# Kernel tuning notes

Measured on AMD Instinct MI355X. Metric: run time of the kernel, lower is better.

The kernel has to match this reference:

```python
import jax, jax.numpy as jnp
import numpy as np

EMB = 1024
HEADS = 16
HEAD_DIM = EMB // HEADS


def setup_inputs() -> dict:
    key = jax.random.key(0)
    ks = jax.random.split(key, 11)
    B, S = 4, 2048
    scale = 1.0 / np.sqrt(EMB)
    inp = {
        "query": jax.random.normal(ks[0], (B, S, EMB), jnp.float32),
        "key": jax.random.normal(ks[1], (B, S, EMB), jnp.float32),
        "value": jax.random.normal(ks[2], (B, S, EMB), jnp.float32),
        "Wq": jax.random.normal(ks[3], (EMB, EMB), jnp.float32) * scale,
        "bq": jnp.zeros((EMB,), jnp.float32),
        "Wk": jax.random.normal(ks[4], (EMB, EMB), jnp.float32) * scale,
        "bk": jnp.zeros((EMB,), jnp.float32),
        "Wv": jax.random.normal(ks[5], (EMB, EMB), jnp.float32) * scale,
        "bv": jnp.zeros((EMB,), jnp.float32),
        "Wo": jax.random.normal(ks[6], (EMB, EMB), jnp.float32) * scale,
        "bo": jnp.zeros((EMB,), jnp.float32),
    }
    return inp


def reference(query, key, value, Wq, bq, Wk, bk, Wv, bv, Wo, bo):
    B, S, E = query.shape
    H, D = HEADS, HEAD_DIM

    def split_heads(x):  # [B,S,E] -> [B,H,S,D]
        return x.reshape(B, -1, H, D).transpose(0, 2, 1, 3)

    Q = split_heads(query @ Wq + bq)
    K = split_heads(key @ Wk + bk)
    V = split_heads(value @ Wv + bv)

    scores = jnp.einsum("bhqd,bhkd->bhqk", Q, K) / jnp.sqrt(jnp.float32(D))
    attn = jax.nn.softmax(scores, axis=-1)
    out = jnp.einsum("bhqk,bhkd->bhqd", attn, V)
    out = out.transpose(0, 2, 1, 3).reshape(B, S, E)
    return out @ Wo + bo
```

## Files before the change

### kernel.cpp

```cpp
#include <hip/hip_runtime.h>

typedef unsigned short ushort_t;
typedef __attribute__((ext_vector_type(8))) short bf16x8;
typedef __attribute__((ext_vector_type(4))) float f32x4;
typedef __attribute__((ext_vector_type(16))) float f32x16;
typedef __attribute__((ext_vector_type(4))) int i32x4;
typedef __attribute__((ext_vector_type(2))) unsigned int u32x2;

#define QSCALE 0.1803368801111204f

__device__ inline ushort_t f2bf(float f) {
    unsigned int u = __float_as_uint(f);
    unsigned int r = (u + 0x7FFFu + ((u >> 16) & 1u)) >> 16;
    return (ushort_t)r;
}
__device__ inline unsigned pkbf(float x, float y) {
    unsigned d;
    asm("v_cvt_pk_bf16_f32 %0, %1, %2" : "=v"(d) : "v"(x), "v"(y));
    return d;
}
__device__ inline bf16x8 frag_from(unsigned a, unsigned b, unsigned c, unsigned d) {
    union { i32x4 i; bf16x8 v; } u;
    u.i[0] = (int)a; u.i[1] = (int)b; u.i[2] = (int)c; u.i[3] = (int)d;
    return u.v;
}

__device__ inline bf16x8 mkfrag(float x0, float x1, float x2, float x3,
                                float x4, float x5, float x6, float x7, int hi) {
    unsigned A_ = pkbf(x0, x1), B_ = pkbf(x2, x3), C_ = pkbf(x4, x5), D_ = pkbf(x6, x7);
    unsigned Ax = (unsigned)__shfl_xor((int)A_, 32);
    unsigned Bx = (unsigned)__shfl_xor((int)B_, 32);
    unsigned Cx = (unsigned)__shfl_xor((int)C_, 32);
    unsigned Dx = (unsigned)__shfl_xor((int)D_, 32);
    return frag_from(hi ? Cx : A_, hi ? Dx : B_, hi ? C_ : Ax, hi ? D_ : Bx);
}

__global__ __launch_bounds__(256) void transpose_cast4(
    const float* __restrict__ W0, const float* __restrict__ W1,
    const float* __restrict__ W2, const float* __restrict__ W3,
    ushort_t* __restrict__ T0, ushort_t* __restrict__ T1,
    ushort_t* __restrict__ T2, ushort_t* __restrict__ T3) {
    __shared__ float tile[32][33];
    const int which = blockIdx.x >> 10;
    const float* W = which == 0 ? W0 : which == 1 ? W1 : which == 2 ? W2 : W3;
    ushort_t* Wt = which == 0 ? T0 : which == 1 ? T1 : which == 2 ? T2 : T3;
    const int bidx = blockIdx.x & 1023;
    const int bx = bidx & 31, by = bidx >> 5;
    const int n0 = bx * 32, k0 = by * 32;
    const int tx = threadIdx.x & 31, ty = threadIdx.x >> 5;
#pragma unroll
    for (int i = 0; i < 4; ++i) {
        int r = ty + i * 8;
        tile[r][tx] = W[(k0 + r) * 1024 + n0 + tx];
    }
    __syncthreads();
#pragma unroll
    for (int i = 0; i < 4; ++i) {
        int r = ty + i * 8;
        Wt[(n0 + r) * 1024 + k0 + tx] = f2bf(tile[tx][r]);
    }
}

__global__ __launch_bounds__(256) void v_transpose(const ushort_t* __restrict__ Vp,
                                                   ushort_t* __restrict__ Vt) {
    __shared__ alignas(16) ushort_t tile[64][72];
    const int bid = blockIdx.x;
    const int pair = bid >> 5, st0 = (bid & 31) * 64;
    const ushort_t* src = Vp + (size_t)pair * 2048 * 64;
    ushort_t* dst = Vt + (size_t)pair * 64 * 2048;
    const int t = threadIdx.x;
    const int sl = t >> 2, d0 = (t & 3) * 16;
    *(bf16x8*)&tile[sl][d0] = *(const bf16x8*)&src[(size_t)(st0 + sl) * 64 + d0];
    *(bf16x8*)&tile[sl][d0 + 8] = *(const bf16x8*)&src[(size_t)(st0 + sl) * 64 + d0 + 8];
    __syncthreads();
    const int dl = t >> 2, s0 = (t & 3) * 16;
    bf16x8 a, b;
#pragma unroll
    for (int j = 0; j < 8; ++j) {
        a[j] = (short)tile[s0 + j][dl];
        b[j] = (short)tile[s0 + 8 + j][dl];
    }
    *(bf16x8*)&dst[(size_t)dl * 2048 + st0 + s0] = a;
    *(bf16x8*)&dst[(size_t)dl * 2048 + st0 + s0 + 8] = b;
}

template <int AF32, int OMODE>
__global__ __launch_bounds__(256) void gemm_bt(const void* __restrict__ Ap,
                                               const ushort_t* __restrict__ Bt,
                                               const float* __restrict__ bias,
                                               void* __restrict__ out, float scale) {
    __shared__ alignas(16) ushort_t As[128 * 72];
    __shared__ alignas(16) ushort_t Bs[128 * 72];
    const int t = threadIdx.x;
    const int lane = t & 63, w = t >> 6;
    const int q = lane & 15, g = lane >> 4;
    const int wr = w >> 1, wc = w & 1;
    const int bm = blockIdx.x & 63, bn = blockIdx.x >> 6;
    const int m0 = bm * 128, n0 = bn * 128;

    f32x4 acc[4][4];
#pragma unroll
    for (int i = 0; i < 4; ++i)
#pragma unroll
        for (int j = 0; j < 4; ++j) acc[i][j] = (f32x4){0.f, 0.f, 0.f, 0.f};

    for (int k0 = 0; k0 < 1024; k0 += 64) {
        __syncthreads();
#pragma unroll
        for (int it = 0; it < 4; ++it) {
            int tt = t + it * 256;
            int row = tt >> 3;
            int col = (tt & 7) * 8;
            if (AF32) {
                const float* A = (const float*)Ap;
                float4 v0 = *(const float4*)&A[(size_t)(m0 + row) * 1024 + k0 + col];
                float4 v1 = *(const float4*)&A[(size_t)(m0 + row) * 1024 + k0 + col + 4];
                *(bf16x8*)&As[row * 72 + col] =
                    frag_from(pkbf(v0.x, v0.y), pkbf(v0.z, v0.w),
                              pkbf(v1.x, v1.y), pkbf(v1.z, v1.w));
            } else {
                const ushort_t* A = (const ushort_t*)Ap;
                *(bf16x8*)&As[row * 72 + col] =
                    *(const bf16x8*)&A[(size_t)(m0 + row) * 1024 + k0 + col];
            }
            *(bf16x8*)&Bs[row * 72 + col] =
                *(const bf16x8*)&Bt[(size_t)(n0 + row) * 1024 + k0 + col];
        }
        __syncthreads();
#pragma unroll
        for (int kt = 0; kt < 2; ++kt) {
            bf16x8 af[4], bfr[4];
#pragma unroll
            for (int mt = 0; mt < 4; ++mt)
                af[mt] = *(const bf16x8*)&As[(wr * 64 + mt * 16 + q) * 72 + kt * 32 + g * 8];
#pragma unroll
            for (int nt = 0; nt < 4; ++nt)
                bfr[nt] = *(const bf16x8*)&Bs[(wc * 64 + nt * 16 + q) * 72 + kt * 32 + g * 8];
#pragma unroll
            for (int mt = 0; mt < 4; ++mt)
#pragma unroll
                for (int nt = 0; nt < 4; ++nt)
                    acc[mt][nt] = __builtin_amdgcn_mfma_f32_16x16x32_bf16(
                        af[mt], bfr[nt], acc[mt][nt], 0, 0, 0);
        }
    }

#pragma unroll
    for (int mt = 0; mt < 4; ++mt) {
#pragma unroll
        for (int nt = 0; nt < 4; ++nt) {
#pragma unroll
            for (int r = 0; r < 4; ++r) {
                int grow = m0 + wr * 64 + mt * 16 + g * 4 + r;
                int col = n0 + wc * 64 + nt * 16 + q;
                float v = acc[mt][nt][r] + bias[col];
                if (OMODE == 0) {
                    int b = grow >> 11, s = grow & 2047;
                    int h = col >> 6, d = col & 63;
                    ((ushort_t*)out)[(((size_t)(b * 16 + h) * 2048 + s) * 64) + d] =
                        f2bf(v * scale);
                } else {
                    ((float*)out)[(size_t)grow * 1024 + col] = v;
                }
            }
        }
    }
}

__global__ __launch_bounds__(512, 4) void attn_kernel(const ushort_t* __restrict__ Qp,
                                                      const ushort_t* __restrict__ Kp,
                                                      const ushort_t* __restrict__ Vtp,
                                                      ushort_t* __restrict__ Oa) {
    __shared__ alignas(16) ushort_t Ks[2][4096];
    __shared__ alignas(16) ushort_t Vs[2][4096];

    const int t = threadIdx.x, lane = t & 63, w = t >> 6;
    const int li = lane & 31, hi = lane >> 5;
    const int bid = (blockIdx.x & 7) * 64 + (blockIdx.x >> 3);
    const int pair = bid >> 3;
    const int qbase = (bid & 7) * 256 + w * 32;

    const ushort_t* Qh = Qp + (size_t)pair * 2048 * 64;
    const ushort_t* Kh = Kp + (size_t)pair * 2048 * 64;
    const ushort_t* Vh = Vtp + (size_t)pair * 64 * 2048;

    bf16x8 qf[4];
#pragma unroll
    for (int ks = 0; ks < 4; ++ks)
        qf[ks] = *(const bf16x8*)&Qh[(size_t)(qbase + li) * 64 + ks * 16 + hi * 8];

    const short one_bf = (short)0x3F80;
    const bf16x8 onesf = {one_bf, one_bf, one_bf, one_bf, one_bf, one_bf, one_bf, one_bf};

    f32x16 o0 = {0.f,0.f,0.f,0.f,0.f,0.f,0.f,0.f,0.f,0.f,0.f,0.f,0.f,0.f,0.f,0.f};
    f32x16 o1 = {0.f,0.f,0.f,0.f,0.f,0.f,0.f,0.f,0.f,0.f,0.f,0.f,0.f,0.f,0.f,0.f};
    f32x16 osum = {0.f,0.f,0.f,0.f,0.f,0.f,0.f,0.f,0.f,0.f,0.f,0.f,0.f,0.f,0.f,0.f};
    float m_ = -1e30f;

    const int r8 = t >> 3;
    const int lcol = (t & 7) * 16;
    const int swoff = (r8 * 128) + (lcol ^ ((r8 & 7) << 4));
    const char* kp0 = (const char*)Kh + (size_t)r8 * 128 + lcol;
    const char* vp0 = (const char*)Vh + (size_t)r8 * 4096 + lcol;
    char* KsB = (char*)Ks;
    char* VsB = (char*)Vs;
    const int sw = (li & 7) << 4;

    i32x4 gk0 = *(const i32x4*)(kp0);
    i32x4 gv0 = *(const i32x4*)(vp0);
    *(i32x4*)(KsB + swoff) = gk0;
    *(i32x4*)(VsB + swoff) = gv0;
    gk0 = *(const i32x4*)(kp0 + 8192);
    gv0 = *(const i32x4*)(vp0 + 128);
    __syncthreads();

    for (int it = 0; it < 32; ++it) {
        const int cur = it & 1;
        if (it < 31) {
            const int nb = (cur ^ 1) * 8192;
            *(i32x4*)(KsB + nb + swoff) = gk0;
            *(i32x4*)(VsB + nb + swoff) = gv0;
        }
        if (it < 30) {
            gk0 = *(const i32x4*)(kp0 + (size_t)(it + 2) * 8192);
            gv0 = *(const i32x4*)(vp0 + (size_t)(it + 2) * 128);
        }

        const char* kb = KsB + cur * 8192;
        const char* vb = VsB + cur * 8192;

        f32x16 s0 = {0.f,0.f,0.f,0.f,0.f,0.f,0.f,0.f,0.f,0.f,0.f,0.f,0.f,0.f,0.f,0.f};
        f32x16 s1 = {0.f,0.f,0.f,0.f,0.f,0.f,0.f,0.f,0.f,0.f,0.f,0.f,0.f,0.f,0.f,0.f};
        __builtin_amdgcn_s_setprio(1);
#pragma unroll
        for (int ks = 0; ks < 4; ++ks) {
            const int b = ks * 32 + hi * 16;
            bf16x8 k0 = *(const bf16x8*)(kb + li * 128 + (b ^ sw));
            bf16x8 k1 = *(const bf16x8*)(kb + (32 + li) * 128 + (b ^ sw));
            s0 = __builtin_amdgcn_mfma_f32_32x32x16_bf16(k0, qf[ks], s0, 0, 0, 0);
            s1 = __builtin_amdgcn_mfma_f32_32x32x16_bf16(k1, qf[ks], s1, 0, 0, 0);
        }
        __builtin_amdgcn_s_setprio(0);

        float mx[8];
#pragma unroll
        for (int j = 0; j < 8; ++j)
            mx[j] = fmaxf(fmaxf(s0[j], s0[j + 8]), fmaxf(s1[j], s1[j + 8]));
        float m01 = fmaxf(mx[0], mx[1]), m23 = fmaxf(mx[2], mx[3]);
        float m45 = fmaxf(mx[4], mx[5]), m67 = fmaxf(mx[6], mx[7]);
        float tm = fmaxf(fmaxf(m01, m23), fmaxf(m45, m67));
        tm = fmaxf(tm, __shfl_xor(tm, 32));
        if (__any(tm > m_ + 8.f)) {
            float mn = fmaxf(m_, tm);
            float corr = exp2f(m_ - mn);
#pragma unroll
            for (int r = 0; r < 16; ++r) { o0[r] *= corr; o1[r] *= corr; }
            osum[0] *= corr;
            m_ = mn;
        }
#pragma unroll
        for (int r = 0; r < 16; ++r) s0[r] = exp2f(s0[r] - m_);
#pragma unroll
        for (int r = 0; r < 16; ++r) s1[r] = exp2f(s1[r] - m_);

        bf16x8 pf[4];
        pf[0] = mkfrag(s0[0], s0[1], s0[2], s0[3], s0[4], s0[5], s0[6], s0[7], hi);
        pf[1] = mkfrag(s0[8], s0[9], s0[10], s0[11], s0[12], s0[13], s0[14], s0[15], hi);
        pf[2] = mkfrag(s1[0], s1[1], s1[2], s1[3], s1[4], s1[5], s1[6], s1[7], hi);
        pf[3] = mkfrag(s1[8], s1[9], s1[10], s1[11], s1[12], s1[13], s1[14], s1[15], hi);

        __builtin_amdgcn_s_setprio(1);
#pragma unroll
        for (int ks = 0; ks < 4; ++ks) {
            const int b = ks * 32 + hi * 16;
            bf16x8 v0 = *(const bf16x8*)(vb + li * 128 + (b ^ sw));
            bf16x8 v1 = *(const bf16x8*)(vb + (32 + li) * 128 + (b ^ sw));
            o0 = __builtin_amdgcn_mfma_f32_32x32x16_bf16(v0, pf[ks], o0, 0, 0, 0);
            o1 = __builtin_amdgcn_mfma_f32_32x32x16_bf16(v1, pf[ks], o1, 0, 0, 0);
            osum = __builtin_amdgcn_mfma_f32_32x32x16_bf16(onesf, pf[ks], osum, 0, 0, 0);
        }
        __builtin_amdgcn_s_setprio(0);

        __syncthreads();
    }

    const float rl = 1.0f / osum[0];
    const int b = pair >> 4, hh = pair & 15;
    const int s = qbase + li;
    const size_t rowbase = ((size_t)(b * 2048 + s)) * 1024 + hh * 64;
#pragma unroll
    for (int dt = 0; dt < 2; ++dt) {
#pragma unroll
        for (int rq = 0; rq < 4; ++rq) {
            float v0 = (dt ? o1[rq * 4 + 0] : o0[rq * 4 + 0]) * rl;
            float v1 = (dt ? o1[rq * 4 + 1] : o0[rq * 4 + 1]) * rl;
            float v2 = (dt ? o1[rq * 4 + 2] : o0[rq * 4 + 2]) * rl;
            float v3 = (dt ? o1[rq * 4 + 3] : o0[rq * 4 + 3]) * rl;
            u32x2 uv;
            uv[0] = pkbf(v0, v1);
            uv[1] = pkbf(v2, v3);
            *(u32x2*)&Oa[rowbase + dt * 32 + rq * 8 + hi * 4] = uv;
        }
    }
}

extern "C" void kernel_launch(void* const* d_in, const int* in_sizes, int n_in,
                              void* d_out, int out_size, void* d_ws, size_t ws_size,
                              hipStream_t stream) {
    const float* query = (const float*)d_in[0];
    const float* key_ = (const float*)d_in[1];
    const float* value = (const float*)d_in[2];
    const float* Wq = (const float*)d_in[3];
    const float* bq = (const float*)d_in[4];
    const float* Wk = (const float*)d_in[5];
    const float* bk = (const float*)d_in[6];
    const float* Wv = (const float*)d_in[7];
    const float* bv = (const float*)d_in[8];
    const float* Wo = (const float*)d_in[9];
    const float* bo = (const float*)d_in[10];
    float* out = (float*)d_out;

    char* ws = (char*)d_ws;
    ushort_t* Wqt = (ushort_t*)(ws + 0);
    ushort_t* Wkt = (ushort_t*)(ws + 2097152);
    ushort_t* Wvt = (ushort_t*)(ws + 4194304);
    ushort_t* Wot = (ushort_t*)(ws + 6291456);
    ushort_t* Qp = (ushort_t*)(ws + 8388608);
    ushort_t* Kp = (ushort_t*)(ws + 25165824);
    ushort_t* Vp = (ushort_t*)(ws + 41943040);
    ushort_t* Vt = (ushort_t*)(ws + 58720256);
    ushort_t* Oa = (ushort_t*)(ws + 41943040);

    transpose_cast4<<<4096, 256, 0, stream>>>(Wq, Wk, Wv, Wo, Wqt, Wkt, Wvt, Wot);

    gemm_bt<1, 0><<<512, 256, 0, stream>>>((const void*)query, Wqt, bq, (void*)Qp, QSCALE);
    gemm_bt<1, 0><<<512, 256, 0, stream>>>((const void*)key_, Wkt, bk, (void*)Kp, 1.0f);
    gemm_bt<1, 0><<<512, 256, 0, stream>>>((const void*)value, Wvt, bv, (void*)Vp, 1.0f);

    v_transpose<<<2048, 256, 0, stream>>>(Vp, Vt);

    attn_kernel<<<512, 512, 0, stream>>>(Qp, Kp, Vt, Oa);

    gemm_bt<0, 1><<<512, 256, 0, stream>>>((const void*)Oa, Wot, bo, (void*)out, 1.0f);
}
```

Measured before the change: 250.9 us.

## Use direct global-to-LDS loads in GEMM and raw v_exp_f32 in attention

The GEMM now loads bf16 operand tiles with global_load_lds straight into unpadded shared memory instead of staging them through registers. The attention kernel swaps exp2f for an inline v_exp_f32, which drops the library's denormal and range handling, and seeds the first score MFMA with a zero constant. Together these aim to cut load instruction overhead, register pressure and exp cost, at the price of LDS bank conflicts from the removed padding and a less exact exp for very small inputs.

```diff
diff --git a/kernel.cpp b/kernel.cpp
--- a/kernel.cpp
+++ b/kernel.cpp
@@ -18,6 +18,11 @@
     unsigned d;
     asm("v_cvt_pk_bf16_f32 %0, %1, %2" : "=v"(d) : "v"(x), "v"(y));
     return d;
+}
+__device__ inline float vexp2(float x) {
+    float r;
+    asm("v_exp_f32 %0, %1" : "=v"(r) : "v"(x));
+    return r;
 }
 __device__ inline bf16x8 frag_from(unsigned a, unsigned b, unsigned c, unsigned d) {
     union { i32x4 i; bf16x8 v; } u;
@@ -89,8 +94,9 @@
                                                const ushort_t* __restrict__ Bt,
                                                const float* __restrict__ bias,
                                                void* __restrict__ out, float scale) {
-    __shared__ alignas(16) ushort_t As[128 * 72];
-    __shared__ alignas(16) ushort_t Bs[128 * 72];
+    constexpr int ASTR = AF32 ? 72 : 64;
+    __shared__ alignas(16) ushort_t As[128 * ASTR];
+    __shared__ alignas(16) ushort_t Bs[128 * 64];
     const int t = threadIdx.x;
     const int lane = t & 63, w = t >> 6;
     const int q = lane & 15, g = lane >> 4;
@@ -98,6 +104,10 @@
     const int bm = blockIdx.x & 63, bn = blockIdx.x >> 6;
     const int m0 = bm * 128, n0 = bn * 128;
 
+    const char* Btc = (const char*)Bt;
+    char* AsB = (char*)As;
+    char* BsB = (char*)Bs;
+
     f32x4 acc[4][4];
 #pragma unroll
     for (int i = 0; i < 4; ++i)
@@ -107,24 +117,36 @@
     for (int k0 = 0; k0 < 1024; k0 += 64) {
         __syncthreads();
 #pragma unroll
-        for (int it = 0; it < 4; ++it) {
-            int tt = t + it * 256;
-            int row = tt >> 3;
-            int col = (tt & 7) * 8;
-            if (AF32) {
-                const float* A = (const float*)Ap;
+        for (int i = 0; i < 4; ++i) {
+            const int c = w * 4 + i;
+            __builtin_amdgcn_global_load_lds(
+                (const __attribute__((address_space(1))) void*)(
+                    Btc + (size_t)(n0 + c * 8 + (lane >> 3)) * 2048 + k0 * 2 + (lane & 7) * 16),
+                (__attribute__((address_space(3))) void*)(BsB + c * 1024), 16, 0, 0);
+        }
+        if (AF32) {
+            const float* A = (const float*)Ap;
+#pragma unroll
+            for (int it = 0; it < 4; ++it) {
+                int tt = t + it * 256;
+                int row = tt >> 3;
+                int col = (tt & 7) * 8;
                 float4 v0 = *(const float4*)&A[(size_t)(m0 + row) * 1024 + k0 + col];
                 float4 v1 = *(const float4*)&A[(size_t)(m0 + row) * 1024 + k0 + col + 4];
-                *(bf16x8*)&As[row * 72 + col] =
+                *(bf16x8*)&As[row * ASTR + col] =
                     frag_from(pkbf(v0.x, v0.y), pkbf(v0.z, v0.w),
                               pkbf(v1.x, v1.y), pkbf(v1.z, v1.w));
-            } else {
-                const ushort_t* A = (const ushort_t*)Ap;
-                *(bf16x8*)&As[row * 72 + col] =
-                    *(const bf16x8*)&A[(size_t)(m0 + row) * 1024 + k0 + col];
             }
-            *(bf16x8*)&Bs[row * 72 + col] =
-                *(const bf16x8*)&Bt[(size_t)(n0 + row) * 1024 + k0 + col];
+        } else {
+            const char* Ac = (const char*)Ap;
+#pragma unroll
+            for (int i = 0; i < 4; ++i) {
+                const int c = w * 4 + i;
+                __builtin_amdgcn_global_load_lds(
+                    (const __attribute__((address_space(1))) void*)(
+                        Ac + (size_t)(m0 + c * 8 + (lane >> 3)) * 2048 + k0 * 2 + (lane & 7) * 16),
+                    (__attribute__((address_space(3))) void*)(AsB + c * 1024), 16, 0, 0);
+            }
         }
         __syncthreads();
 #pragma unroll
@@ -132,10 +154,10 @@
             bf16x8 af[4], bfr[4];
 #pragma unroll
             for (int mt = 0; mt < 4; ++mt)
-                af[mt] = *(const bf16x8*)&As[(wr * 64 + mt * 16 + q) * 72 + kt * 32 + g * 8];
+                af[mt] = *(const bf16x8*)&As[(wr * 64 + mt * 16 + q) * ASTR + kt * 32 + g * 8];
 #pragma unroll
             for (int nt = 0; nt < 4; ++nt)
-                bfr[nt] = *(const bf16x8*)&Bs[(wc * 64 + nt * 16 + q) * 72 + kt * 32 + g * 8];
+                bfr[nt] = *(const bf16x8*)&Bs[(wc * 64 + nt * 16 + q) * 64 + kt * 32 + g * 8];
 #pragma unroll
             for (int mt = 0; mt < 4; ++mt)
 #pragma unroll
@@ -191,10 +213,9 @@
 
     const short one_bf = (short)0x3F80;
     const bf16x8 onesf = {one_bf, one_bf, one_bf, one_bf, one_bf, one_bf, one_bf, one_bf};
-
-    f32x16 o0 = {0.f,0.f,0.f,0.f,0.f,0.f,0.f,0.f,0.f,0.f,0.f,0.f,0.f,0.f,0.f,0.f};
-    f32x16 o1 = {0.f,0.f,0.f,0.f,0.f,0.f,0.f,0.f,0.f,0.f,0.f,0.f,0.f,0.f,0.f,0.f};
-    f32x16 osum = {0.f,0.f,0.f,0.f,0.f,0.f,0.f,0.f,0.f,0.f,0.f,0.f,0.f,0.f,0.f,0.f};
+    const f32x16 z16 = {0.f,0.f,0.f,0.f,0.f,0.f,0.f,0.f,0.f,0.f,0.f,0.f,0.f,0.f,0.f,0.f};
+
+    f32x16 o0 = z16, o1 = z16, osum = z16;
     float m_ = -1e30f;
 
     const int r8 = t >> 3;
@@ -229,11 +250,17 @@
         const char* kb = KsB + cur * 8192;
         const char* vb = VsB + cur * 8192;
 
-        f32x16 s0 = {0.f,0.f,0.f,0.f,0.f,0.f,0.f,0.f,0.f,0.f,0.f,0.f,0.f,0.f,0.f,0.f};
-        f32x16 s1 = {0.f,0.f,0.f,0.f,0.f,0.f,0.f,0.f,0.f,0.f,0.f,0.f,0.f,0.f,0.f,0.f};
+        f32x16 s0, s1;
         __builtin_amdgcn_s_setprio(1);
-#pragma unroll
-        for (int ks = 0; ks < 4; ++ks) {
+        {
+            const int b = hi * 16;
+            bf16x8 k0 = *(const bf16x8*)(kb + li * 128 + (b ^ sw));
+            bf16x8 k1 = *(const bf16x8*)(kb + (32 + li) * 128 + (b ^ sw));
+            s0 = __builtin_amdgcn_mfma_f32_32x32x16_bf16(k0, qf[0], z16, 0, 0, 0);
+            s1 = __builtin_amdgcn_mfma_f32_32x32x16_bf16(k1, qf[0], z16, 0, 0, 0);
+        }
+#pragma unroll
+        for (int ks = 1; ks < 4; ++ks) {
             const int b = ks * 32 + hi * 16;
             bf16x8 k0 = *(const bf16x8*)(kb + li * 128 + (b ^ sw));
             bf16x8 k1 = *(const bf16x8*)(kb + (32 + li) * 128 + (b ^ sw));
@@ -252,16 +279,16 @@
         tm = fmaxf(tm, __shfl_xor(tm, 32));
         if (__any(tm > m_ + 8.f)) {
             float mn = fmaxf(m_, tm);
-            float corr = exp2f(m_ - mn);
+            float corr = vexp2(m_ - mn);
 #pragma unroll
             for (int r = 0; r < 16; ++r) { o0[r] *= corr; o1[r] *= corr; }
             osum[0] *= corr;
             m_ = mn;
         }
 #pragma unroll
-        for (int r = 0; r < 16; ++r) s0[r] = exp2f(s0[r] - m_);
-#pragma unroll
-        for (int r = 0; r < 16; ++r) s1[r] = exp2f(s1[r] - m_);
+        for (int r = 0; r < 16; ++r) s0[r] = vexp2(s0[r] - m_);
+#pragma unroll
+        for (int r = 0; r < 16; ++r) s1[r] = vexp2(s1[r] - m_);
 
         bf16x8 pf[4];
         pf[0] = mkfrag(s0[0], s0[1], s0[2], s0[3], s0[4], s0[5], s0[6], s0[7], hi);
```

New measurement: 244.1 us. 1.03x faster.
